# Performance work log

Measured on AMD Instinct MI355X. Metric: run time of the kernel, lower is better.

## Reference

```python
import jax, jax.numpy as jnp
import numpy as np

B = 8
C = 128          # channels
H = 1024         # sparse (hidden) channels in bottleneck
START = 128      # start_frames
SPARSE = 8192    # sparse_frames
K = 512          # k_sparse
N_UP = 6         # log2(SPARSE/START) upsample blocks
EPS = 1e-5


def conv1d(x, w, b, stride=1, pad=0):
    # x: (B, Cin, L), w: (Cout, Cin, K)
    y = jax.lax.conv_general_dilated(
        x, w, window_strides=(stride,), padding=[(pad, pad)],
        dimension_numbers=('NCW', 'OIW', 'NCW'))
    return y + b[None, :, None]


def batch_norm(x, g, beta):
    # training-mode BatchNorm1d: stats over (batch, length) per channel
    m = x.mean(axis=(0, 2), keepdims=True)
    v = x.var(axis=(0, 2), keepdims=True)
    return (x - m) * jax.lax.rsqrt(v + EPS) * g[None, :, None] + beta[None, :, None]


def lrelu(x):
    return jnp.where(x >= 0, x, 0.2 * x)


def setup_inputs() -> dict:
    key = jax.random.key(0)
    ks = jax.random.split(key, 16)
    s = 0.05
    return {
        'x': jax.random.normal(ks[0], (B, C, START), dtype=jnp.float32),
        'up_w': jax.random.normal(ks[1], (N_UP, C, C, 3), dtype=jnp.float32) * s,
        'up_b': jnp.zeros((N_UP, C), dtype=jnp.float32),
        'up_g': jnp.ones((N_UP, C), dtype=jnp.float32),
        'up_beta': jnp.zeros((N_UP, C), dtype=jnp.float32),
        'up_out_w': jax.random.normal(ks[2], (C, C, 3), dtype=jnp.float32) * s,
        'up_out_b': jnp.zeros((C,), dtype=jnp.float32),
        # SparseBottleneck 1x1 convs (stored as (out,in) matrices)
        'sb_up_w': jax.random.normal(ks[3], (H, C), dtype=jnp.float32) * s,
        'sb_up_b': jnp.zeros((H,), dtype=jnp.float32),
        'sal_w': jax.random.normal(ks[4], (H, C), dtype=jnp.float32) * s,
        'sal_b': jnp.zeros((H,), dtype=jnp.float32),
        'sb_down_w': jax.random.normal(ks[5], (C, H), dtype=jnp.float32) * s,
        'sb_down_b': jnp.zeros((C,), dtype=jnp.float32),
        'dn_w': jax.random.normal(ks[6], (3, C, C, 7), dtype=jnp.float32) * s,
        'dn_b': jnp.zeros((3, C), dtype=jnp.float32),
        'dn_g': jnp.ones((3, C), dtype=jnp.float32),
        'dn_beta': jnp.zeros((3, C), dtype=jnp.float32),
    }


def reference(x, up_w, up_b, up_g, up_beta, up_out_w, up_out_b,
              sb_up_w, sb_up_b, sal_w, sal_b, sb_down_w, sb_down_b,
              dn_w, dn_b, dn_g, dn_beta):
    # ---- ConvUpsample: 128 -> 8192 frames ----
    for i in range(N_UP):
        x = jnp.repeat(x, 2, axis=-1)
        x = conv1d(x, up_w[i], up_b[i], stride=1, pad=1)
        x = lrelu(batch_norm(x, up_g[i], up_beta[i]))
    x = conv1d(x, up_out_w, up_out_b, stride=1, pad=1)  # (B, C, 8192)

    # ---- SparseBottleneck ----
    sig = jnp.einsum('bcl,hc->bhl', x, sb_up_w) + sb_up_b[None, :, None]   # (B,H,L)
    sal = jnp.einsum('bcl,hc->bhl', x, sal_w) + sal_b[None, :, None]       # (B,H,L)
    flat = jax.nn.softmax(sal.reshape(B, -1), axis=-1)   # softmax over H*L
    vals, idx = jax.lax.top_k(flat, K)                   # (B, K)
    sparse = jnp.zeros_like(flat).at[jnp.arange(B)[:, None], idx].set(vals)
    sal = sparse.reshape(sal.shape)
    x = sig * sal                                         # gated, (B,H,L)
    x = jnp.einsum('bhl,ch->bcl', x, sb_down_w) + sb_down_b[None, :, None]

    # ---- down stack: 8192 -> 128 frames ----
    for i in range(3):
        x = conv1d(x, dn_w[i], dn_b[i], stride=4, pad=3)
        x = lrelu(x)
        x = batch_norm(x, dn_g[i], dn_beta[i])
    return x  # (B, C, 128)
```

## Files before the change

### kernel.cpp

```cpp
#include <hip/hip_runtime.h>
#include <hip/hip_bf16.h>


#define DEV_INLINE __device__ __forceinline__

constexpr int NB   = 8;
constexpr int NC   = 128;
constexpr int NH   = 1024;
constexpr int LFULL= 8192;
constexpr int KSEL = 512;
constexpr int CAP  = 32768;

typedef __attribute__((ext_vector_type(4))) float f32x4;
typedef __attribute__((ext_vector_type(8))) short bf16x8;

DEV_INLINE unsigned monoKey(float f) {
    unsigned u = __float_as_uint(f);
    return (u & 0x80000000u) ? ~u : (u | 0x80000000u);
}
DEV_INLINE float keyToF(unsigned k) {
    unsigned u = (k & 0x80000000u) ? (k ^ 0x80000000u) : ~k;
    return __uint_as_float(u);
}
DEV_INLINE unsigned monoKey16(unsigned u) {
    return (u & 0x8000u) ? ((~u) & 0xFFFFu) : (u | 0x8000u);
}
DEV_INLINE unsigned bf16r(float f) {
    unsigned u = __float_as_uint(f);
    return (u + 0x7FFFu + ((u >> 16) & 1u)) >> 16;
}
DEV_INLINE float lrelu(float v) { return v >= 0.f ? v : 0.2f * v; }
DEV_INLINE float f4c(const float4& v, int k) {
    return k == 0 ? v.x : k == 1 ? v.y : k == 2 ? v.z : v.w;
}
DEV_INLINE int swz4(int p) { return p ^ ((p >> 3) & 7); }

DEV_INLINE void loadg4(const float* __restrict__ rowp, int g0, int L, float* e) {
    if (g0 >= 0 && g0 + 4 <= L) {
        float4 v = *(const float4*)(rowp + g0);
        e[0] = v.x; e[1] = v.y; e[2] = v.z; e[3] = v.w;
    } else {
#pragma unroll
        for (int t = 0; t < 4; t++) {
            int g = g0 + t;
            e[t] = (g >= 0 && g < L) ? rowp[g] : 0.f;
        }
    }
}

__global__ __launch_bounds__(256) void prep_k(
    const float* __restrict__ up_w, const float* __restrict__ up_out_w,
    const float* __restrict__ dn_w, float* __restrict__ wprep)
{
    int idx = blockIdx.x * 256 + threadIdx.x;
    if (idx < 393216) {
        int layer = idx >> 16;
        int r0 = idx & 65535;
        int c = r0 >> 9, r = (r0 >> 7) & 3, o = r0 & 127;
        const float* wsrc = up_w + ((size_t)layer * 128 + o) * 384 + c * 3;
        float w0 = wsrc[0], w1 = wsrc[1], w2 = wsrc[2];
        wprep[idx] = (r == 0) ? w0 : (r == 1) ? (w1 + w2) : (r == 2) ? (w0 + w1) : w2;
    } else if (idx < 442368) {
        int r0 = idx - 393216;
        int c = r0 / 384, k = (r0 / 128) % 3, o = r0 & 127;
        wprep[idx] = up_out_w[((size_t)o * 128 + c) * 3 + k];
    } else {
        int r0 = idx - 442368;
        int layer = r0 / 114688;
        int r1 = r0 - layer * 114688;
        int c = r1 / 896, k = (r1 / 128) % 7, o = r1 & 127;
        wprep[idx] = dn_w[((size_t)layer * 128 + o) * 896 + c * 7 + k];
    }
}

__global__ __launch_bounds__(256) void prepA_k(
    const float* __restrict__ up_w, const float* __restrict__ up_out_w,
    unsigned short* __restrict__ afrag)
{
    int idx = blockIdx.x * 256 + threadIdx.x;
    if (idx >= 221184) return;
    int rid = idx >> 6, lane = idx & 63;
    const int r15 = lane & 15, g = lane >> 4;
    unsigned short vals[8];
    if (rid < 3072) {
        int L  = rid >> 9;
        int r0 = rid & 511;
        int f = r0 & 3, ks = (r0 >> 2) & 1, cc = (r0 >> 3) & 1;
        int wo = (r0 >> 4) & 1, half = (r0 >> 5) & 1, ptap = (r0 >> 6) & 3;
        int o = wo * 64 + f * 16 + r15;
        int cb = cc * 64 + ks * 32 + g * 8;
#pragma unroll
        for (int e = 0; e < 8; e++) {
            const float* ws = up_w + (((size_t)L * 128 + o) * 128 + (cb + e)) * 3;
            float w0 = ws[0], w1 = ws[1], w2 = ws[2];
            float v = (ptap == 0) ? w0 : (ptap == 1) ? (w1 + w2)
                    : (ptap == 2) ? (w0 + w1) : w2;
            unsigned hi = bf16r(v);
            if (half == 0) vals[e] = (unsigned short)hi;
            else vals[e] = (unsigned short)bf16r(v - __uint_as_float(hi << 16));
        }
    } else {
        int r2 = rid - 3072;
        int f = r2 & 3, ks = (r2 >> 2) & 1, cc = (r2 >> 3) & 1;
        int wo = (r2 >> 4) & 1, half = (r2 >> 5) & 1, tap = r2 >> 6;
        int o = wo * 64 + f * 16 + r15;
        int cb = cc * 64 + ks * 32 + g * 8;
#pragma unroll
        for (int e = 0; e < 8; e++) {
            float v = up_out_w[((size_t)o * 128 + (cb + e)) * 3 + tap];
            unsigned hi = bf16r(v);
            if (half == 0) vals[e] = (unsigned short)hi;
            else vals[e] = (unsigned short)bf16r(v - __uint_as_float(hi << 16));
        }
    }
    unsigned pk[4];
#pragma unroll
    for (int q = 0; q < 4; q++)
        pk[q] = (unsigned)vals[2*q] | ((unsigned)vals[2*q+1] << 16);
    *(uint4*)(afrag + (size_t)rid * 512 + lane * 8) = make_uint4(pk[0], pk[1], pk[2], pk[3]);
}

__global__ __launch_bounds__(256) void redstats_k(
    const float* __restrict__ partial, int nb, float* __restrict__ stats)
{
    const int c = threadIdx.x;
    float s0 = 0.f, s1 = 0.f, s2 = 0.f, s3 = 0.f;
    for (int i = blockIdx.x * 4; i < nb; i += gridDim.x * 4) {
        s0 += partial[(size_t)(i + 0) * 256 + c];
        s1 += partial[(size_t)(i + 1) * 256 + c];
        s2 += partial[(size_t)(i + 2) * 256 + c];
        s3 += partial[(size_t)(i + 3) * 256 + c];
    }
    float s = (s0 + s1) + (s2 + s3);
    if (s != 0.f || blockIdx.x == 0) atomicAdd(&stats[c], s);
}

template<int INMODE>
__global__ __launch_bounds__(512) void mconvU_k(
    const float* __restrict__ in, float* __restrict__ out,
    const unsigned short* __restrict__ afrag, const float* __restrict__ bias,
    const float* __restrict__ stp, const float* __restrict__ gp,
    const float* __restrict__ btp, float inv_n,
    float* __restrict__ partial, int L_in)
{
    __shared__ unsigned short Xh[66 * 64], Xl[66 * 64];
    __shared__ float scs[NC], shs[NC];
    __shared__ float sstat[256];

    const int b = blockIdx.y, tile0 = blockIdx.x * 64, tid = threadIdx.x;
    const int lane = tid & 63, wid = tid >> 6;
    const int wo = wid >> 2, par = (wid >> 1) & 1, jh = wid & 1;
    const int r15 = lane & 15, g = lane >> 4;
    const int bid = b * gridDim.x + blockIdx.x;

    if (tid < 256) sstat[tid] = 0.f;
    if (INMODE > 0) {
        for (int c = tid; c < NC; c += 512) {
            float m  = stp[c] * inv_n;
            float va = stp[NC + c] * inv_n - m * m;
            float sc = gp[c] * rsqrtf(va + 1e-5f);
            scs[c] = sc;
            shs[c] = btp[c] - m * sc;
        }
    }

    f32x4 acc[4][2];
#pragma unroll
    for (int i = 0; i < 4; i++)
#pragma unroll
        for (int j = 0; j < 2; j++) acc[i][j] = (f32x4)(0.f);

    for (int cc = 0; cc < 2; cc++) {
        __syncthreads();
        {
            int r = tid & 63;
            int l = tile0 - 1 + r;
            for (int c0 = (tid >> 6); c0 < 64; c0 += 8) {
                int c = cc * 64 + c0;
                float v = 0.f;
                if (l >= 0 && l < L_in) {
                    v = in[((size_t)b * NC + c) * L_in + l];
                    if (INMODE > 0) v = lrelu(v * scs[c] + shs[c]);
                }
                unsigned hi = bf16r(v);
                unsigned lo = bf16r(v - __uint_as_float(hi << 16));
                unsigned bo = ((unsigned)(r * 128 + c0 * 2)) ^ (((unsigned)(r & 7)) << 4);
                *(unsigned short*)((char*)Xh + bo) = (unsigned short)hi;
                *(unsigned short*)((char*)Xl + bo) = (unsigned short)lo;
            }
            if (tid < 128) {
                int r2 = 64 + (tid >> 6);
                int l2 = tile0 - 1 + r2;
                int c0 = tid & 63;
                int c = cc * 64 + c0;
                float v = 0.f;
                if (l2 >= 0 && l2 < L_in) {
                    v = in[((size_t)b * NC + c) * L_in + l2];
                    if (INMODE > 0) v = lrelu(v * scs[c] + shs[c]);
                }
                unsigned hi = bf16r(v);
                unsigned lo = bf16r(v - __uint_as_float(hi << 16));
                unsigned bo = ((unsigned)(r2 * 128 + c0 * 2)) ^ (((unsigned)(r2 & 7)) << 4);
                *(unsigned short*)((char*)Xh + bo) = (unsigned short)hi;
                *(unsigned short*)((char*)Xl + bo) = (unsigned short)lo;
            }
        }
        __syncthreads();
#pragma unroll
        for (int pt = 0; pt < 2; pt++) {
            const int ptap = par * 2 + pt;
            const int roff = (ptap == 0) ? 0 : (ptap == 3) ? 2 : 1;
#pragma unroll
            for (int combo = 0; combo < 3; combo++) {
                const int ah = (combo == 2) ? 1 : 0;
                const unsigned short* Xs = (combo == 1) ? Xl : Xh;
                bf16x8 af[8];
#pragma unroll
                for (int ks = 0; ks < 2; ks++)
#pragma unroll
                    for (int f = 0; f < 4; f++) {
                        int rec = ((((ptap * 2 + ah) * 2 + wo) * 2 + cc) * 2 + ks) * 4 + f;
                        af[ks * 4 + f] = *(const bf16x8*)(afrag + (size_t)rec * 512 + lane * 8);
                    }
#pragma unroll
                for (int ks = 0; ks < 2; ks++) {
                    bf16x8 bf_[2];
#pragma unroll
                    for (int j = 0; j < 2; j++) {
                        int row = (jh * 2 + j) * 16 + r15 + roff;
                        unsigned bo = ((unsigned)(row * 128 + ks * 64 + g * 16))
                                    ^ (((unsigned)(row & 7)) << 4);
                        bf_[j] = *(const bf16x8*)((const char*)Xs + bo);
                    }
#pragma unroll
                    for (int i = 0; i < 4; i++)
#pragma unroll
                        for (int j = 0; j < 2; j++)
                            acc[i][j] = __builtin_amdgcn_mfma_f32_16x16x32_bf16(
                                af[ks * 4 + i], bf_[j], acc[i][j], 0, 0, 0);
                }
            }
        }
    }

    const int L_out = 2 * L_in;
#pragma unroll
    for (int i = 0; i < 4; i++) {
#pragma unroll
        for (int r = 0; r < 4; r++) {
            const int o = wo * 64 + i * 16 + g * 4 + r;
            const float bv = bias[o];
            float s1 = 0.f, s2 = 0.f;
#pragma unroll
            for (int j = 0; j < 2; j++) {
                float v = acc[i][j][r] + bv;
                int lout = 2 * (tile0 + (jh * 2 + j) * 16 + r15) + par;
                out[((size_t)b * NC + o) * L_out + lout] = v;
                s1 += v; s2 += v * v;
            }
#pragma unroll
            for (int m = 1; m < 16; m <<= 1) {
                s1 += __shfl_xor(s1, m);
                s2 += __shfl_xor(s2, m);
            }
            if (r15 == 0) {
                atomicAdd(&sstat[o], s1);
                atomicAdd(&sstat[NC + o], s2);
            }
        }
    }
    __syncthreads();
    if (tid < 256) partial[(size_t)bid * 256 + tid] = sstat[tid];
}

__global__ __launch_bounds__(512) void mconvF_k(
    const float* __restrict__ in, float* __restrict__ out,
    const unsigned short* __restrict__ afrag, const float* __restrict__ bias,
    const float* __restrict__ stp, const float* __restrict__ gp,
    const float* __restrict__ btp, float inv_n,
    unsigned short* __restrict__ xtout)
{
    __shared__ unsigned short Xh[130 * 64], Xl[130 * 64];
    __shared__ float scs[NC], shs[NC];

    const int b = blockIdx.y, l0 = blockIdx.x * 128, tid = threadIdx.x;
    const int lane = tid & 63, wid = tid >> 6;
    const int wo = wid >> 2, wl = (wid & 3) * 32;
    const int r15 = lane & 15, g = lane >> 4;

    for (int c = tid; c < NC; c += 512) {
        float m  = stp[c] * inv_n;
        float va = stp[NC + c] * inv_n - m * m;
        float sc = gp[c] * rsqrtf(va + 1e-5f);
        scs[c] = sc;
        shs[c] = btp[c] - m * sc;
    }

    f32x4 acc[4][2];
#pragma unroll
    for (int i = 0; i < 4; i++)
#pragma unroll
        for (int j = 0; j < 2; j++) acc[i][j] = (f32x4)(0.f);

    for (int cc = 0; cc < 2; cc++) {
        __syncthreads();
        {
            int r = tid & 127;
            int l = l0 - 1 + r;
            for (int c0 = (tid >> 7); c0 < 64; c0 += 4) {
                int c = cc * 64 + c0;
                float v = 0.f;
                if (l >= 0 && l < LFULL) {
                    v = in[((size_t)b * NC + c) * LFULL + l];
                    v = lrelu(v * scs[c] + shs[c]);
                }
                unsigned hi = bf16r(v);
                unsigned lo = bf16r(v - __uint_as_float(hi << 16));
                unsigned bo = ((unsigned)(r * 128 + c0 * 2)) ^ (((unsigned)(r & 7)) << 4);
                *(unsigned short*)((char*)Xh + bo) = (unsigned short)hi;
                *(unsigned short*)((char*)Xl + bo) = (unsigned short)lo;
            }
            if (tid < 128) {
                int r2 = 128 + (tid >> 6);
                int l2 = l0 - 1 + r2;
                int c0 = tid & 63;
                int c = cc * 64 + c0;
                float v = 0.f;
                if (l2 >= 0 && l2 < LFULL) {
                    v = in[((size_t)b * NC + c) * LFULL + l2];
                    v = lrelu(v * scs[c] + shs[c]);
                }
                unsigned hi = bf16r(v);
                unsigned lo = bf16r(v - __uint_as_float(hi << 16));
                unsigned bo = ((unsigned)(r2 * 128 + c0 * 2)) ^ (((unsigned)(r2 & 7)) << 4);
                *(unsigned short*)((char*)Xh + bo) = (unsigned short)hi;
                *(unsigned short*)((char*)Xl + bo) = (unsigned short)lo;
            }
        }
        __syncthreads();
#pragma unroll
        for (int tap = 0; tap < 3; tap++) {
#pragma unroll
            for (int combo = 0; combo < 3; combo++) {
                const int ah = (combo == 2) ? 1 : 0;
                const unsigned short* Xs = (combo == 1) ? Xl : Xh;
                bf16x8 af[8];
#pragma unroll
                for (int ks = 0; ks < 2; ks++)
#pragma unroll
                    for (int f = 0; f < 4; f++) {
                        int rec = 3072 + ((((tap * 2 + ah) * 2 + wo) * 2 + cc) * 2 + ks) * 4 + f;
                        af[ks * 4 + f] = *(const bf16x8*)(afrag + (size_t)rec * 512 + lane * 8);
                    }
#pragma unroll
                for (int ks = 0; ks < 2; ks++) {
                    bf16x8 bf_[2];
#pragma unroll
                    for (int j = 0; j < 2; j++) {
                        int row = wl + j * 16 + r15 + tap;
                        unsigned bo = ((unsigned)(row * 128 + ks * 64 + g * 16))
                                    ^ (((unsigned)(row & 7)) << 4);
                        bf_[j] = *(const bf16x8*)((const char*)Xs + bo);
                    }
#pragma unroll
                    for (int i = 0; i < 4; i++)
#pragma unroll
                        for (int j = 0; j < 2; j++)
                            acc[i][j] = __builtin_amdgcn_mfma_f32_16x16x32_bf16(
                                af[ks * 4 + i], bf_[j], acc[i][j], 0, 0, 0);
                }
            }
        }
    }

#pragma unroll
    for (int i = 0; i < 4; i++) {
#pragma unroll
        for (int r = 0; r < 4; r++) {
            const int o = wo * 64 + i * 16 + g * 4 + r;
            const float bv = bias[o];
#pragma unroll
            for (int j = 0; j < 2; j++) {
                float v = acc[i][j][r] + bv;
                int l = l0 + wl + j * 16 + r15;
                out[((size_t)b * NC + o) * LFULL + l] = v;
                xtout[((size_t)b * LFULL + l) * NC + o] = (unsigned short)bf16r(v);
            }
        }
    }
}

template<int KW, int STRIDE, int PAD, bool UPS, int INMODE, bool OUTACT, bool STATS, int TT, bool XPOSE, int OCW>
__global__ __launch_bounds__(256) void conv7_k(
    const float* __restrict__ in, float* __restrict__ out,
    const float* __restrict__ wp, const float* __restrict__ bias,
    const float* __restrict__ stp, const float* __restrict__ gp,
    const float* __restrict__ btp, float inv_n,
    float* __restrict__ stats, unsigned short* __restrict__ xtout,
    int L_in, int L_out)
{
    constexpr int CC    = (KW == 7) ? 8 : 16;
    constexpr int PT    = 64 * TT;
    constexpr int TTO   = UPS ? 2 * TT : TT;
    constexpr int NWR   = UPS ? 4 : KW;
    constexpr int OCB   = 4 * OCW;
    constexpr int SPAN  = UPS ? (PT + 2) : ((PT - 1) * STRIDE + KW);
    constexpr int NCH   = (SPAN + 3) / 4;
    constexpr int NCH8  = (NCH + 7) & ~7;
    constexpr int XROW  = 4 * NCH8 + 4;
    constexpr int NLD   = (CC * NCH + 255) / 256;
    constexpr int XSPAN = UPS ? (TT + 2) : ((TT - 1) * STRIDE + KW);
    constexpr int STEP  = UPS ? TT : TT * STRIDE;
    constexpr int NWQ   = CC * NWR * (OCB / 4);
    static_assert((STEP & 3) == 0, "conv7 swizzle path requires STEP%4==0");
    static_assert(OCW == 4 || OCW == 8, "OCW must be 4 or 8");

    __shared__ float xs[CC][XROW];
    __shared__ float wls[CC * NWR * OCB];
    __shared__ float scs[NC], shs[NC];

    const int b = blockIdx.z, ocb = blockIdx.y, tid = threadIdx.x;
    const int t0 = blockIdx.x * PT, lane = tid & 63;
    const int wid = tid >> 6;
    const int oc0 = ocb * OCB + wid * OCW;
    const int gb = UPS ? (t0 - 1) : (t0 * STRIDE - PAD);

    if (INMODE > 0) {
        for (int c = tid; c < NC; c += 256) {
            float m  = stp[c] * inv_n;
            float va = stp[NC + c] * inv_n - m * m;
            float sc = gp[c] * rsqrtf(va + 1e-5f);
            scs[c] = sc;
            shs[c] = btp[c] - m * sc;
        }
        __syncthreads();
    }

    float acc[OCW][TTO];
#pragma unroll
    for (int i = 0; i < OCW; i++)
#pragma unroll
        for (int j = 0; j < TTO; j++) acc[i][j] = 0.f;

    float pre[NLD][4];

#define C7_STAGEW(CCBASE) do {                                              \
    for (int _u = tid; _u < NWQ; _u += 256) {                               \
        int _row = _u / (OCB / 4), _g8 = _u % (OCB / 4);                    \
        int _cl = _row / NWR, _t = _row % NWR;                              \
        ((float4*)wls)[_u] = *(const float4*)(wp +                          \
            ((size_t)((CCBASE) + _cl) * NWR + _t) * 128 + ocb * OCB + _g8 * 4); \
    }                                                                       \
} while (0)

#define C7_COMPCI(CI) do {                                                  \
    float _q[XSPAN];                                                        \
    const int _qb4 = lane * (STEP / 4);                                     \
    _Pragma("unroll")                                                       \
    for (int _u = 0; _u < XSPAN / 4; _u++) {                                \
        float4 _v = *(const float4*)&xs[CI][4 * swz4(_qb4 + _u)];           \
        _q[4*_u] = _v.x; _q[4*_u+1] = _v.y;                                 \
        _q[4*_u+2] = _v.z; _q[4*_u+3] = _v.w;                               \
    }                                                                       \
    if constexpr ((XSPAN & 3) != 0) {                                       \
        const int _pt = swz4(_qb4 + XSPAN / 4);                             \
        if constexpr ((XSPAN & 3) >= 2) {                                   \
            float2 _v = *(const float2*)&xs[CI][4 * _pt];                   \
            _q[(XSPAN & ~3)] = _v.x; _q[(XSPAN & ~3) + 1] = _v.y;           \
        }                                                                   \
        if constexpr ((XSPAN & 3) == 1)                                     \
            _q[XSPAN - 1] = xs[CI][4 * _pt];                                \
        else if constexpr ((XSPAN & 3) == 3)                                \
            _q[XSPAN - 1] = xs[CI][4 * _pt + 2];                            \
    }                                                                       \
    {                                                                       \
        _Pragma("unroll")                                                   \
        for (int _k = 0; _k < KW; _k++) {                                   \
            if constexpr (OCW == 8) {                                       \
                const float4 _w0 = *(const float4*)&wls[((CI) * NWR + _k) * OCB + wid * 8];     \
                const float4 _w1 = *(const float4*)&wls[((CI) * NWR + _k) * OCB + wid * 8 + 4]; \
                _Pragma("unroll")                                           \
                for (int _i = 0; _i < 8; _i++) {                            \
                    float _wv = f4c(_i < 4 ? _w0 : _w1, _i & 3);            \
                    _Pragma("unroll")                                       \
                    for (int _j = 0; _j < TT; _j++)                         \
                        acc[_i][_j] = fmaf(_wv, _q[_j * STRIDE + _k], acc[_i][_j]); \
                }                                                           \
            } else {                                                        \
                const float4 _w0 = *(const float4*)&wls[((CI) * NWR + _k) * OCB + wid * 4];     \
                _Pragma("unroll")                                           \
                for (int _i = 0; _i < 4; _i++) {                            \
                    float _wv = f4c(_w0, _i);                               \
                    _Pragma("unroll")                                       \
                    for (int _j = 0; _j < TT; _j++)                         \
                        acc[_i][_j] = fmaf(_wv, _q[_j * STRIDE + _k], acc[_i][_j]); \
                }                                                           \
            }                                                               \
        }                                                                   \
    }                                                                       \
} while (0)

#pragma unroll
    for (int u = 0; u < NLD; u++) {
        int idx = tid + u * 256;
        if (idx < CC * NCH) {
            int cl = idx / NCH, q = idx - cl * NCH;
            loadg4(in + ((size_t)b * NC + cl) * L_in, gb + 4 * q, L_in, pre[u]);
        }
    }
#pragma unroll
    for (int u = 0; u < NLD; u++) {
        int idx = tid + u * 256;
        if (idx < CC * NCH) {
            int cl = idx / NCH, q = idx - cl * NCH;
            int g0 = gb + 4 * q;
            float e[4];
#pragma unroll
            for (int t = 0; t < 4; t++) {
                float v = pre[u][t];
                if (INMODE > 0) {
                    int gg = g0 + t;
                    if (gg >= 0 && gg < L_in) {
                        float s = v * scs[cl] + shs[cl];
                        v = (INMODE == 2) ? lrelu(s) : s;
                    }
                }
                e[t] = v;
            }
            *(float4*)&xs[cl][4 * swz4(q)] = make_float4(e[0], e[1], e[2], e[3]);
        }
    }
    C7_STAGEW(0);
    __syncthreads();

    for (int cc = 0; cc < NC; cc += CC) {
        if (cc + CC < NC) {
#pragma unroll
            for (int u = 0; u < NLD; u++) {
                int idx = tid + u * 256;
                if (idx < CC * NCH) {
                    int cl = idx / NCH, q = idx - cl * NCH;
                    loadg4(in + ((size_t)b * NC + cc + CC + cl) * L_in,
                           gb + 4 * q, L_in, pre[u]);
                }
            }
        }
#pragma unroll
        for (int ci = 0; ci < CC; ci++) {
            C7_COMPCI(ci);
        }
        __syncthreads();
        if (cc + CC < NC) {
#pragma unroll
            for (int u = 0; u < NLD; u++) {
                int idx = tid + u * 256;
                if (idx < CC * NCH) {
                    int cl = idx / NCH, q = idx - cl * NCH;
                    int g0 = gb + 4 * q;
                    int c = cc + CC + cl;
                    float e[4];
#pragma unroll
                    for (int t = 0; t < 4; t++) {
                        float v = pre[u][t];
                        if (INMODE > 0) {
                            int gg = g0 + t;
                            if (gg >= 0 && gg < L_in) {
                                float s = v * scs[c] + shs[c];
                                v = (INMODE == 2) ? lrelu(s) : s;
                            }
                        }
                        e[t] = v;
                    }
                    *(float4*)&xs[cl][4 * swz4(q)] = make_float4(e[0], e[1], e[2], e[3]);
                }
            }
            C7_STAGEW(cc + CC);
            __syncthreads();
        }
    }
#undef C7_STAGEW
#undef C7_COMPCI

    const int po = t0 + lane * TTO;
#pragma unroll
    for (int i = 0; i < OCW; i++) {
        const int o = oc0 + i;
        const float bv = bias[o];
        float s1 = 0.f, s2 = 0.f;
        float tmpm[TTO];
#pragma unroll
        for (int j = 0; j < TTO; j++) {
            float v = acc[i][j] + bv;
            if (OUTACT) v = lrelu(v);
            tmpm[j] = v;
            if (STATS) { s1 += v; s2 += v * v; }
        }
        float* orow = out + ((size_t)b * NC + o) * L_out + po;
        if constexpr (TTO == 4)
            *(float4*)orow = make_float4(tmpm[0], tmpm[1], tmpm[2], tmpm[3]);
        else if constexpr (TTO == 2)
            *(float2*)orow = make_float2(tmpm[0], tmpm[1]);
        else
            orow[0] = tmpm[0];
        if (STATS) {
#pragma unroll
            for (int m = 1; m < 64; m <<= 1) {
                s1 += __shfl_xor(s1, m);
                s2 += __shfl_xor(s2, m);
            }
            if (lane == 0) {
                atomicAdd(&stats[o], s1);
                atomicAdd(&stats[NC + o], s2);
            }
        }
    }
}

__global__ __launch_bounds__(256) void cvtW_k(const float* __restrict__ W,
                                              unsigned short* __restrict__ Wbf)
{
    int i = blockIdx.x * 256 + threadIdx.x;
    const float4 a = *(const float4*)&W[i * 8];
    const float4 b = *(const float4*)&W[i * 8 + 4];
    unsigned pk[4];
    pk[0] = bf16r(a.x) | (bf16r(a.y) << 16);
    pk[1] = bf16r(a.z) | (bf16r(a.w) << 16);
    pk[2] = bf16r(b.x) | (bf16r(b.y) << 16);
    pk[3] = bf16r(b.z) | (bf16r(b.w) << 16);
    *(uint4*)&Wbf[i * 8] = make_uint4(pk[0], pk[1], pk[2], pk[3]);
}

template<int PHASE>
__global__ __launch_bounds__(256) void salM2_k(
    const unsigned short* __restrict__ xT, const unsigned short* __restrict__ Wbf,
    const float* __restrict__ bias, float* __restrict__ gsum,
    unsigned* __restrict__ ghist, const unsigned* __restrict__ thrv,
    unsigned* __restrict__ candcnt, unsigned* __restrict__ candI)
{
    __shared__ unsigned short Bls[128 * 128];
    __shared__ float redsm[4];

    const int b  = blockIdx.z;
    const int h0 = blockIdx.y * 128;
    const int l0 = blockIdx.x * 128;
    const int tid = threadIdx.x;
    const int lane = tid & 63;
    const int wid = tid >> 6;
    const int wh = (wid >> 1) * 64;
    const int wl = (wid & 1) * 64;
    const int r15 = lane & 15, g = lane >> 4;

    unsigned thr = 0;
    if (PHASE == 1) thr = thrv[b * 2];

    bf16x8 af[4][4];
#pragma unroll
    for (int ks = 0; ks < 4; ks++)
#pragma unroll
        for (int f = 0; f < 4; f++) {
            int row = h0 + wh + f * 16 + r15;
            af[ks][f] = *(const bf16x8*)(Wbf + (size_t)row * NC + ks * 32 + g * 8);
        }

    {
        const uint4* gB = (const uint4*)(xT + ((size_t)b * LFULL + l0) * NC);
        char* cB = (char*)Bls;
        for (int i = tid; i < 2048; i += 256) {
            int row = i >> 4, q = i & 15;
            unsigned sw = (unsigned)(row * 256 + q * 16) ^ (((unsigned)(row & 7)) << 4);
            *(uint4*)(cB + sw) = gB[i];
        }
    }
    __syncthreads();

    f32x4 acc[4][4];
#pragma unroll
    for (int i = 0; i < 4; i++)
#pragma unroll
        for (int j = 0; j < 4; j++) acc[i][j] = (f32x4)(0.f);

#pragma unroll
    for (int ks = 0; ks < 4; ks++) {
        bf16x8 bfv[4];
#pragma unroll
        for (int f = 0; f < 4; f++) {
            int rowB = wl + f * 16 + r15;
            unsigned offB = (unsigned)(rowB * 256 + ks * 64 + g * 16)
                          ^ (((unsigned)(rowB & 7)) << 4);
            bfv[f] = *(const bf16x8*)((const char*)Bls + offB);
        }
#pragma unroll
        for (int i = 0; i < 4; i++)
#pragma unroll
            for (int j = 0; j < 4; j++)
                acc[i][j] = __builtin_amdgcn_mfma_f32_16x16x32_bf16(
                    af[ks][i], bfv[j], acc[i][j], 0, 0, 0);
    }

    if constexpr (PHASE == 0) {
        __syncthreads();
        unsigned* lhist = (unsigned*)Bls;
        for (int i = tid; i < 8192; i += 256) lhist[i] = 0;
        __syncthreads();
        unsigned* myh = lhist + (tid & 1) * 4096;
        float expsum = 0.f;
#pragma unroll
        for (int i = 0; i < 4; i++) {
#pragma unroll
            for (int r = 0; r < 4; r++) {
                const int h = h0 + wh + i * 16 + g * 4 + r;
                const float bv = bias[h];
#pragma unroll
                for (int j = 0; j < 4; j++) {
                    float v = acc[i][j][r] + bv;
                    expsum += __expf(v);
                    atomicAdd(&myh[monoKey16(bf16r(v)) >> 4], 1u);
                }
            }
        }
#pragma unroll
        for (int m = 1; m < 64; m <<= 1) expsum += __shfl_xor(expsum, m);
        if (lane == 0) redsm[wid] = expsum;
        __syncthreads();
        for (int i = tid; i < 4096; i += 256) {
            unsigned s = lhist[i] + lhist[4096 + i];
            if (s) atomicAdd(&ghist[b * 4096 + i], s);
        }
        if (tid == 0)
            atomicAdd(&gsum[b], redsm[0] + redsm[1] + redsm[2] + redsm[3]);
    } else {
#pragma unroll
        for (int i = 0; i < 4; i++) {
#pragma unroll
            for (int r = 0; r < 4; r++) {
                const int h = h0 + wh + i * 16 + g * 4 + r;
                const float bv = bias[h];
#pragma unroll
                for (int j = 0; j < 4; j++) {
                    float v = acc[i][j][r] + bv;
                    bool pr = monoKey16(bf16r(v)) >= thr;
                    unsigned long long m = __ballot(pr);
                    if (m) {
                        int leader = __ffsll((unsigned long long)m) - 1;
                        int cnt = __popcll(m);
                        unsigned basepos = 0;
                        if (lane == leader)
                            basepos = atomicAdd(&candcnt[b], (unsigned)cnt);
                        basepos = __shfl(basepos, leader);
                        if (pr) {
                            int rr = __popcll(m & ((1ull << lane) - 1ull));
                            unsigned pos = basepos + (unsigned)rr;
                            if (pos < CAP) {
                                int l = l0 + wl + j * 16 + r15;
                                candI[b * CAP + pos] = (unsigned)((h << 13) | l);
                            }
                        }
                    }
                }
            }
        }
    }
}

__global__ __launch_bounds__(256) void scan2_k(
    const unsigned* __restrict__ ghist, unsigned* __restrict__ thrv)
{
    const int b = blockIdx.x, tid = threadIdx.x;
    __shared__ unsigned part[256];
    unsigned s = 0;
#pragma unroll
    for (int i = 0; i < 16; i++) s += ghist[b * 4096 + tid * 16 + i];
    part[tid] = s;
    __syncthreads();
    if (tid == 0) {
        unsigned cum = 0; int ch;
        for (ch = 255; ch >= 0; ch--) {
            if (cum + part[ch] >= KSEL) break;
            cum += part[ch];
        }
        int bin = 0;
        if (ch >= 0) {
            for (bin = ch * 16 + 15; bin > ch * 16; bin--) {
                unsigned c = ghist[b * 4096 + bin];
                if (cum + c >= KSEL) break;
                cum += c;
            }
        }
        int bcol = bin > 0 ? bin - 1 : 0;
        thrv[b * 2] = (unsigned)bcol << 4;
    }
}

__global__ __launch_bounds__(128) void recompute_k(
    const unsigned* __restrict__ candcnt, const unsigned* __restrict__ candI,
    const float* __restrict__ xu, const float* __restrict__ W,
    const float* __restrict__ bias, unsigned* __restrict__ candK)
{
    const int b = blockIdx.y;
    const unsigned cnt = min(candcnt[b], (unsigned)CAP);
    const int t = threadIdx.x;
    __shared__ float wsum[2];
    for (unsigned k = blockIdx.x; k < cnt; k += 1024) {
        unsigned e = candI[b * CAP + k];
        int h = e >> 13, l = e & 8191;
        float prod = W[h * NC + t] * xu[(b * NC + t) * LFULL + l];
#pragma unroll
        for (int m = 1; m < 64; m <<= 1) prod += __shfl_xor(prod, m);
        if ((t & 63) == 0) wsum[t >> 6] = prod;
        __syncthreads();
        if (t == 0) candK[b * CAP + k] = monoKey(wsum[0] + wsum[1] + bias[h]);
        __syncthreads();
    }
}

__global__ __launch_bounds__(256) void select2_k(
    const unsigned* __restrict__ candcnt, const unsigned* __restrict__ candK,
    const unsigned* __restrict__ candI,
    uint2* __restrict__ selected, unsigned* __restrict__ selcnt)
{
    const int b = blockIdx.x, tid = threadIdx.x;
    __shared__ unsigned h1[4096];
    __shared__ unsigned l2k[2048], l2i[2048];
    __shared__ unsigned part[256];
    __shared__ unsigned sh[8];

    const unsigned Nc = min(candcnt[b], (unsigned)CAP);
    const unsigned* kk = candK + b * CAP;
    const unsigned* ii = candI + b * CAP;
    uint2* sel = selected + b * KSEL;

    for (int i = tid; i < 4096; i += 256) h1[i] = 0;
    if (tid < 8) sh[tid] = 0;
    __syncthreads();
    for (unsigned i = tid; i < Nc; i += 256) atomicAdd(&h1[kk[i] >> 20], 1u);
    __syncthreads();
    {
        unsigned s = 0;
#pragma unroll
        for (int i = 0; i < 16; i++) s += h1[tid * 16 + i];
        part[tid] = s;
        __syncthreads();
        if (tid == 0) {
            unsigned cum = 0; int ch;
            for (ch = 255; ch >= 0; ch--) { if (cum + part[ch] >= KSEL) break; cum += part[ch]; }
            int bin = 0;
            if (ch >= 0)
                for (bin = ch * 16 + 15; bin > ch * 16; bin--) {
                    unsigned c = h1[bin];
                    if (cum + c >= KSEL) break;
                    cum += c;
                }
            sh[2] = (unsigned)bin; sh[3] = KSEL - cum;
        }
    }
    __syncthreads();
    const unsigned b1 = sh[2], need1 = sh[3];
    for (int i = tid; i < 1024; i += 256) h1[i] = 0;
    __syncthreads();
    for (unsigned i = tid; i < Nc; i += 256) {
        unsigned k = kk[i], bin = k >> 20;
        if (bin > b1) {
            unsigned p = atomicAdd(&sh[0], 1u);
            if (p < KSEL) sel[p] = make_uint2(k, ii[i]);
        } else if (bin == b1) {
            atomicAdd(&h1[(k >> 10) & 1023], 1u);
        }
    }
    __syncthreads();
    {
        unsigned s = 0;
#pragma unroll
        for (int i = 0; i < 4; i++) s += h1[tid * 4 + i];
        part[tid] = s;
        __syncthreads();
        if (tid == 0) {
            unsigned cum = 0; int ch;
            for (ch = 255; ch >= 0; ch--) { if (cum + part[ch] >= need1) break; cum += part[ch]; }
            int bin = 0;
            if (ch >= 0)
                for (bin = ch * 4 + 3; bin > ch * 4; bin--) {
                    unsigned c = h1[bin];
                    if (cum + c >= need1) break;
                    cum += c;
                }
            sh[4] = (unsigned)bin; sh[5] = need1 - cum;
        }
    }
    __syncthreads();
    const unsigned b2 = sh[4], need2 = sh[5];
    for (int i = tid; i < 1024; i += 256) h1[i] = 0;
    __syncthreads();
    for (unsigned i = tid; i < Nc; i += 256) {
        unsigned k = kk[i];
        if ((k >> 20) != b1) continue;
        unsigned mb = (k >> 10) & 1023;
        if (mb > b2) {
            unsigned p = atomicAdd(&sh[0], 1u);
            if (p < KSEL) sel[p] = make_uint2(k, ii[i]);
        } else if (mb == b2) {
            unsigned j = atomicAdd(&sh[1], 1u);
            if (j < 2048) { l2k[j] = k; l2i[j] = ii[i]; atomicAdd(&h1[k & 1023], 1u); }
        }
    }
    __syncthreads();
    const unsigned m2 = min(sh[1], 2048u);
    {
        unsigned s = 0;
#pragma unroll
        for (int i = 0; i < 4; i++) s += h1[tid * 4 + i];
        part[tid] = s;
        __syncthreads();
        if (tid == 0) {
            unsigned cum = 0; int ch;
            for (ch = 255; ch >= 0; ch--) { if (cum + part[ch] >= need2) break; cum += part[ch]; }
            int bin = 0;
            if (ch >= 0)
                for (bin = ch * 4 + 3; bin > ch * 4; bin--) {
                    unsigned c = h1[bin];
                    if (cum + c >= need2) break;
                    cum += c;
                }
            sh[6] = (unsigned)bin; sh[7] = need2 - cum;
        }
    }
    __syncthreads();
    const unsigned b3 = sh[6], need3 = sh[7];
    if (tid == 0) sh[1] = 0;
    __syncthreads();
    for (unsigned i = tid; i < m2; i += 256) {
        unsigned k = l2k[i], lb = k & 1023;
        if (lb > b3) {
            unsigned p = atomicAdd(&sh[0], 1u);
            if (p < KSEL) sel[p] = make_uint2(k, l2i[i]);
        } else if (lb == b3) {
            unsigned t = atomicAdd(&sh[1], 1u);
            if (t < need3) {
                unsigned p = atomicAdd(&sh[0], 1u);
                if (p < KSEL) sel[p] = make_uint2(k, l2i[i]);
            }
        }
    }
    __syncthreads();
    if (tid == 0) selcnt[b] = min(sh[0], (unsigned)KSEL);
}

__global__ __launch_bounds__(128) void scatter2_k(
    const uint2* __restrict__ selected, const unsigned* __restrict__ selcnt,
    const float* __restrict__ gsum, const float* __restrict__ xu,
    const float* __restrict__ upw, const float* __restrict__ upb,
    float* __restrict__ gval)
{
    const int b = blockIdx.y, kidx = blockIdx.x;
    if (kidx >= (int)selcnt[b]) return;
    const uint2 s = selected[b * KSEL + kidx];
    const float salv = keyToF(s.x);
    const unsigned idx = s.y;
    const int h = idx >> 13, l = idx & 8191;
    const int t = threadIdx.x;

    float prod = upw[h * NC + t] * xu[(b * NC + t) * LFULL + l];
#pragma unroll
    for (int m = 1; m < 64; m <<= 1) prod += __shfl_xor(prod, m);
    __shared__ float wsum[2];
    if ((t & 63) == 0) wsum[t >> 6] = prod;
    __syncthreads();
    if (t == 0) {
        const float sig = wsum[0] + wsum[1] + upb[h];
        gval[b * KSEL + kidx] = sig * (__expf(salv) / gsum[b]);
    }
}

__global__ __launch_bounds__(128) void dnconst_k(
    const float* __restrict__ dn_w, const float* __restrict__ dnb,
    const float* __restrict__ dn_b0, float* __restrict__ cst)
{
    const int o = threadIdx.x;
    float accA = 0.f, accE = 0.f;
    for (int c = 0; c < NC; c++) {
        const float bv = dnb[c];
        const float* wp = dn_w + ((size_t)o * NC + c) * 7;
#pragma unroll
        for (int k = 0; k < 7; k++) {
            float w = wp[k];
            accA += w * bv;
            if (k >= 3) accE += w * bv;
        }
    }
    cst[o]       = accA + dn_b0[o];
    cst[NC + o]  = accE + dn_b0[o];
}

__global__ __launch_bounds__(256) void fillpre_k(
    const float* __restrict__ cst, float* __restrict__ pre)
{
    const int row = blockIdx.x;
    const int o = row & 127;
    const float vI = cst[o], v0 = cst[NC + o];
    float4* p = (float4*)(pre + (size_t)row * 2048);
#pragma unroll
    for (int u = 0; u < 2; u++) {
        int q = threadIdx.x + u * 256;
        float4 v = make_float4(vI, vI, vI, vI);
        if (q == 0) v.x = v0;
        p[q] = v;
    }
}

__global__ __launch_bounds__(128) void corrdn_k(
    const uint2* __restrict__ selected, const unsigned* __restrict__ selcnt,
    const float* __restrict__ gval, const float* __restrict__ dww,
    const float* __restrict__ w0p, float* __restrict__ pre)
{
    const int b = blockIdx.y, kidx = blockIdx.x;
    if (kidx >= (int)selcnt[b]) return;
    const unsigned idx = selected[b * KSEL + kidx].y;
    const int h = idx >> 13, l = idx & 8191;
    const float g = gval[b * KSEL + kidx];
    const int o = threadIdx.x;

    __shared__ float dlt[NC];
    dlt[o] = dww[o * NH + h] * g;
    __syncthreads();

    const int tlo = (l <= 3) ? 0 : ((l - 3 + 3) >> 2);
    const int thi = min(2047, (l + 3) >> 2);
    for (int t = tlo; t <= thi; t++) {
        const int k = l - 4 * t + 3;
        float corr = 0.f;
#pragma unroll 4
        for (int c = 0; c < NC; c++)
            corr += w0p[(size_t)c * 896 + k * 128 + o] * dlt[c];
        atomicAdd(&pre[((size_t)b * NC + o) * 2048 + t], corr);
    }
}

__global__ __launch_bounds__(256) void actstats_k(
    float* __restrict__ pre, float* __restrict__ stats)
{
    const int row = blockIdx.x;
    const int o = row & 127;
    float4* p = (float4*)(pre + (size_t)row * 2048);
    float s1 = 0.f, s2 = 0.f;
#pragma unroll
    for (int u = 0; u < 2; u++) {
        int q = threadIdx.x + u * 256;
        float4 v = p[q];
        float e[4] = {v.x, v.y, v.z, v.w};
#pragma unroll
        for (int t = 0; t < 4; t++) {
            float a = lrelu(e[t]);
            e[t] = a;
            s1 += a; s2 += a * a;
        }
        p[q] = make_float4(e[0], e[1], e[2], e[3]);
    }
#pragma unroll
    for (int m = 1; m < 64; m <<= 1) {
        s1 += __shfl_xor(s1, m);
        s2 += __shfl_xor(s2, m);
    }
    __shared__ float red[8];
    const int lane = threadIdx.x & 63, wid = threadIdx.x >> 6;
    if (lane == 0) { red[wid] = s1; red[4 + wid] = s2; }
    __syncthreads();
    if (threadIdx.x == 0) {
        atomicAdd(&stats[o],      red[0] + red[1] + red[2] + red[3]);
        atomicAdd(&stats[NC + o], red[4] + red[5] + red[6] + red[7]);
    }
}

__global__ void apply_k(const float* __restrict__ in, const float* __restrict__ stats,
                        const float* __restrict__ g, const float* __restrict__ bt,
                        float* __restrict__ out, float inv_n)
{
    int i = blockIdx.x * 256 + threadIdx.x;
    int c = (i >> 7) & 127;
    float m  = stats[c] * inv_n;
    float va = stats[NC + c] * inv_n - m * m;
    float sc = g[c] * rsqrtf(va + 1e-5f);
    out[i] = in[i] * sc + (bt[c] - m * sc);
}

extern "C" void kernel_launch(void* const* d_in, const int* in_sizes, int n_in,
                              void* d_out, int out_size, void* d_ws, size_t ws_size,
                              hipStream_t stream)
{
    const float* x        = (const float*)d_in[0];
    const float* up_w     = (const float*)d_in[1];
    const float* up_b     = (const float*)d_in[2];
    const float* up_g     = (const float*)d_in[3];
    const float* up_beta  = (const float*)d_in[4];
    const float* up_out_w = (const float*)d_in[5];
    const float* up_out_b = (const float*)d_in[6];
    const float* sb_up_w  = (const float*)d_in[7];
    const float* sb_up_b  = (const float*)d_in[8];
    const float* sal_w    = (const float*)d_in[9];
    const float* sal_b    = (const float*)d_in[10];
    const float* sb_dn_w  = (const float*)d_in[11];
    const float* sb_dn_b  = (const float*)d_in[12];
    const float* dn_w     = (const float*)d_in[13];
    const float* dn_b     = (const float*)d_in[14];
    const float* dn_g     = (const float*)d_in[15];
    const float* dn_beta  = (const float*)d_in[16];

    char* ws = (char*)d_ws;
    float*          stats    = (float*)(ws + 0);
    float*          gsum     = (float*)(ws + 16384);
    unsigned*       thrv     = (unsigned*)(ws + 16416);
    unsigned*       candcnt  = (unsigned*)(ws + 16480);
    unsigned*       selcnt   = (unsigned*)(ws + 16512);
    uint2*          selected = (uint2*)(ws + 16640);
    unsigned*       ghist    = (unsigned*)(ws + 49408);
    unsigned*       candK    = (unsigned*)(ws + 180480);
    unsigned*       candI    = (unsigned*)(ws + 1229056);
    unsigned short* Wbf      = (unsigned short*)(ws + 2277632);
    float*          wprep    = (float*)(ws + 2539776);
    float*          B0       = (float*)(ws + 5685504);
    float*          B1       = (float*)(ws + 39239936);
    unsigned short* xT       = (unsigned short*)(ws + 72794368);
    unsigned short* Afrag    = (unsigned short*)(ws + 117440512);
    float*          partial  = (float*)(ws + 121634816);
    float*          gval     = (float*)(ws + 122159104);
    float*          cst      = (float*)(ws + 122175488);

    hipMemsetAsync(d_ws, 0, 16544, stream);
    hipMemsetAsync(ws + 49408, 0, 131072, stream);

    cvtW_k<<<64,256,0,stream>>>(sal_w, Wbf);
    prep_k<<<3072,256,0,stream>>>(up_w, up_out_w, dn_w, wprep);
    prepA_k<<<864,256,0,stream>>>(up_w, up_out_w, Afrag);

    mconvU_k<0><<<dim3(2,NB),512,0,stream>>>(
        x, B0, Afrag, up_b, nullptr, nullptr, nullptr, 0.f, partial, 128);
    redstats_k<<<16,256,0,stream>>>(partial, 2*NB, stats);
    mconvU_k<2><<<dim3(4,NB),512,0,stream>>>(
        B0, B1, Afrag + 1*262144, up_b + NC,
        stats, up_g, up_beta, 1.f/(float)(NB*256), partial, 256);
    redstats_k<<<16,256,0,stream>>>(partial, 4*NB, stats + 256);
    mconvU_k<2><<<dim3(8,NB),512,0,stream>>>(
        B1, B0, Afrag + 2*262144, up_b + 2*NC,
        stats + 256, up_g + NC, up_beta + NC, 1.f/(float)(NB*512), partial, 512);
    redstats_k<<<16,256,0,stream>>>(partial, 8*NB, stats + 2*256);
    mconvU_k<2><<<dim3(16,NB),512,0,stream>>>(
        B0, B1, Afrag + 3*262144, up_b + 3*NC,
        stats + 2*256, up_g + 2*NC, up_beta + 2*NC, 1.f/(float)(NB*1024), partial, 1024);
    redstats_k<<<16,256,0,stream>>>(partial, 16*NB, stats + 3*256);
    mconvU_k<2><<<dim3(32,NB),512,0,stream>>>(
        B1, B0, Afrag + 4*262144, up_b + 4*NC,
        stats + 3*256, up_g + 3*NC, up_beta + 3*NC, 1.f/(float)(NB*2048), partial, 2048);
    redstats_k<<<16,256,0,stream>>>(partial, 32*NB, stats + 4*256);
    mconvU_k<2><<<dim3(64,NB),512,0,stream>>>(
        B0, B1, Afrag + 5*262144, up_b + 5*NC,
        stats + 4*256, up_g + 4*NC, up_beta + 4*NC, 1.f/(float)(NB*4096), partial, 4096);
    redstats_k<<<16,256,0,stream>>>(partial, 64*NB, stats + 5*256);
    mconvF_k<<<dim3(64,NB),512,0,stream>>>(
        B1, B0, Afrag, up_out_b,
        stats + 5*256, up_g + 5*NC, up_beta + 5*NC, 1.f/(float)(NB*LFULL), xT);

    salM2_k<0><<<dim3(64,8,NB),256,0,stream>>>(xT, Wbf, sal_b, gsum, ghist,
                                               nullptr, nullptr, nullptr);
    scan2_k<<<NB,256,0,stream>>>(ghist, thrv);
    salM2_k<1><<<dim3(64,8,NB),256,0,stream>>>(xT, Wbf, sal_b, nullptr, nullptr,
                                               thrv, candcnt, candI);
    recompute_k<<<dim3(1024,NB),128,0,stream>>>(candcnt, candI, B0, sal_w, sal_b, candK);
    select2_k<<<NB,256,0,stream>>>(candcnt, candK, candI, selected, selcnt);
    scatter2_k<<<dim3(KSEL,NB),128,0,stream>>>(selected, selcnt, gsum, B0,
                                               sb_up_w, sb_up_b, gval);

    dnconst_k<<<1,128,0,stream>>>(dn_w, sb_dn_b, dn_b, cst);
    fillpre_k<<<NB*NC,256,0,stream>>>(cst, B1);
    corrdn_k<<<dim3(KSEL,NB),128,0,stream>>>(selected, selcnt, gval, sb_dn_w,
                                             wprep + 442368, B1);
    actstats_k<<<NB*NC,256,0,stream>>>(B1, stats + 6*256);

    conv7_k<7,4,3,false,1,true,true,1,false,4><<<dim3(8,8,NB),256,0,stream>>>(
        B1, B0, wprep + 442368 + 114688, dn_b + NC,
        stats + 6*256, dn_g, dn_beta, 1.f/(float)(NB*2048),
        stats + 7*256, nullptr, 2048, 512);
    conv7_k<7,4,3,false,1,true,true,1,false,4><<<dim3(2,8,NB),256,0,stream>>>(
        B0, B1, wprep + 442368 + 2*114688, dn_b + 2*NC,
        stats + 7*256, dn_g + NC, dn_beta + NC, 1.f/(float)(NB*512),
        stats + 8*256, nullptr, 512, 128);

    apply_k<<<(out_size + 255)/256,256,0,stream>>>(
        B1, stats + 8*256, dn_g + 2*NC, dn_beta + 2*NC, (float*)d_out,
        1.f/(float)(NB*128));
}
```

Baseline: 649.1 us.

## Replace second saliency GEMM pass with per-tile local top-K candidate buffering

The saliency GEMM used to run twice: once for the histogram and softmax sum, then again to collect candidates above the global threshold. Now each tile builds its own histogram, picks a tile-local threshold that keeps at least K entries, and stores those keyed candidates in a per-tile buffer. A light filter kernel then applies the global threshold to the buffered entries instead of recomputing the GEMM. This adds per-tile shared-memory scans and extra global writes, and a tile that overflows its TCAP buffer can silently drop candidates.

```diff
diff --git a/kernel.cpp b/kernel.cpp
--- a/kernel.cpp
+++ b/kernel.cpp
@@ -10,6 +10,7 @@
 constexpr int LFULL= 8192;
 constexpr int KSEL = 512;
 constexpr int CAP  = 32768;
+constexpr int TCAP = 2048;
 
 typedef __attribute__((ext_vector_type(4))) float f32x4;
 typedef __attribute__((ext_vector_type(8))) short bf16x8;
@@ -630,15 +631,16 @@
     *(uint4*)&Wbf[i * 8] = make_uint4(pk[0], pk[1], pk[2], pk[3]);
 }
 
-template<int PHASE>
-__global__ __launch_bounds__(256) void salM2_k(
+__global__ __launch_bounds__(256) void salM3_k(
     const unsigned short* __restrict__ xT, const unsigned short* __restrict__ Wbf,
     const float* __restrict__ bias, float* __restrict__ gsum,
-    unsigned* __restrict__ ghist, const unsigned* __restrict__ thrv,
-    unsigned* __restrict__ candcnt, unsigned* __restrict__ candI)
+    unsigned* __restrict__ ghist, unsigned* __restrict__ tcand,
+    unsigned* __restrict__ tcnt)
 {
     __shared__ unsigned short Bls[128 * 128];
     __shared__ float redsm[4];
+    __shared__ unsigned part[256];
+    __shared__ unsigned shv[2];
 
     const int b  = blockIdx.z;
     const int h0 = blockIdx.y * 128;
@@ -649,9 +651,7 @@
     const int wh = (wid >> 1) * 64;
     const int wl = (wid & 1) * 64;
     const int r15 = lane & 15, g = lane >> 4;
-
-    unsigned thr = 0;
-    if (PHASE == 1) thr = thrv[b * 2];
+    const int tileid = (b * 8 + blockIdx.y) * 64 + blockIdx.x;
 
     bf16x8 af[4][4];
 #pragma unroll
@@ -697,65 +697,130 @@
                     af[ks][i], bfv[j], acc[i][j], 0, 0, 0);
     }
 
-    if constexpr (PHASE == 0) {
-        __syncthreads();
-        unsigned* lhist = (unsigned*)Bls;
-        for (int i = tid; i < 8192; i += 256) lhist[i] = 0;
-        __syncthreads();
-        unsigned* myh = lhist + (tid & 1) * 4096;
-        float expsum = 0.f;
-#pragma unroll
-        for (int i = 0; i < 4; i++) {
-#pragma unroll
-            for (int r = 0; r < 4; r++) {
-                const int h = h0 + wh + i * 16 + g * 4 + r;
-                const float bv = bias[h];
-#pragma unroll
-                for (int j = 0; j < 4; j++) {
-                    float v = acc[i][j][r] + bv;
-                    expsum += __expf(v);
-                    atomicAdd(&myh[monoKey16(bf16r(v)) >> 4], 1u);
-                }
-            }
-        }
-#pragma unroll
-        for (int m = 1; m < 64; m <<= 1) expsum += __shfl_xor(expsum, m);
-        if (lane == 0) redsm[wid] = expsum;
-        __syncthreads();
-        for (int i = tid; i < 4096; i += 256) {
-            unsigned s = lhist[i] + lhist[4096 + i];
-            if (s) atomicAdd(&ghist[b * 4096 + i], s);
-        }
-        if (tid == 0)
-            atomicAdd(&gsum[b], redsm[0] + redsm[1] + redsm[2] + redsm[3]);
-    } else {
-#pragma unroll
-        for (int i = 0; i < 4; i++) {
-#pragma unroll
-            for (int r = 0; r < 4; r++) {
-                const int h = h0 + wh + i * 16 + g * 4 + r;
-                const float bv = bias[h];
-#pragma unroll
-                for (int j = 0; j < 4; j++) {
-                    float v = acc[i][j][r] + bv;
-                    bool pr = monoKey16(bf16r(v)) >= thr;
-                    unsigned long long m = __ballot(pr);
-                    if (m) {
-                        int leader = __ffsll((unsigned long long)m) - 1;
-                        int cnt = __popcll(m);
-                        unsigned basepos = 0;
-                        if (lane == leader)
-                            basepos = atomicAdd(&candcnt[b], (unsigned)cnt);
-                        basepos = __shfl(basepos, leader);
-                        if (pr) {
-                            int rr = __popcll(m & ((1ull << lane) - 1ull));
-                            unsigned pos = basepos + (unsigned)rr;
-                            if (pos < CAP) {
-                                int l = l0 + wl + j * 16 + r15;
-                                candI[b * CAP + pos] = (unsigned)((h << 13) | l);
-                            }
+    __syncthreads();
+    unsigned* hA = (unsigned*)Bls;
+    for (int i = tid; i < 8192; i += 256) hA[i] = 0;
+    if (tid < 2) shv[tid] = 0;
+    __syncthreads();
+    unsigned* myh = hA + (tid & 1) * 4096;
+    float expsum = 0.f;
+#pragma unroll
+    for (int i = 0; i < 4; i++) {
+#pragma unroll
+        for (int r = 0; r < 4; r++) {
+            const int h = h0 + wh + i * 16 + g * 4 + r;
+            const float bv = bias[h];
+#pragma unroll
+            for (int j = 0; j < 4; j++) {
+                float v = acc[i][j][r] + bv;
+                expsum += __expf(v);
+                atomicAdd(&myh[monoKey16(bf16r(v)) >> 4], 1u);
+            }
+        }
+    }
+#pragma unroll
+    for (int m = 1; m < 64; m <<= 1) expsum += __shfl_xor(expsum, m);
+    if (lane == 0) redsm[wid] = expsum;
+    __syncthreads();
+    for (int i = tid; i < 4096; i += 256) {
+        unsigned s = hA[i] + hA[4096 + i];
+        hA[i] = s;
+        if (s) atomicAdd(&ghist[b * 4096 + i], s);
+    }
+    __syncthreads();
+    {
+        unsigned s = 0;
+#pragma unroll
+        for (int i = 0; i < 16; i++) s += hA[tid * 16 + i];
+        part[tid] = s;
+    }
+    __syncthreads();
+    if (tid == 0) {
+        atomicAdd(&gsum[b], redsm[0] + redsm[1] + redsm[2] + redsm[3]);
+        unsigned cum = 0; int ch;
+        for (ch = 255; ch >= 0; ch--) {
+            if (cum + part[ch] >= KSEL) break;
+            cum += part[ch];
+        }
+        int bin = 0;
+        if (ch >= 0) {
+            for (bin = ch * 16 + 15; bin > ch * 16; bin--) {
+                unsigned c = hA[bin];
+                if (cum + c >= KSEL) break;
+                cum += c;
+            }
+        }
+        shv[0] = (unsigned)(bin > 0 ? bin - 1 : 0) << 4;
+    }
+    __syncthreads();
+    const unsigned lthr = shv[0];
+    unsigned* tc = tcand + (size_t)tileid * TCAP;
+#pragma unroll
+    for (int i = 0; i < 4; i++) {
+#pragma unroll
+        for (int r = 0; r < 4; r++) {
+            const int hl = wh + i * 16 + g * 4 + r;
+            const float bv = bias[h0 + hl];
+#pragma unroll
+            for (int j = 0; j < 4; j++) {
+                float v = acc[i][j][r] + bv;
+                unsigned k16 = monoKey16(bf16r(v));
+                bool pr = k16 >= lthr;
+                unsigned long long m = __ballot(pr);
+                if (m) {
+                    int leader = __ffsll((unsigned long long)m) - 1;
+                    int cnt = __popcll(m);
+                    unsigned base = 0;
+                    if (lane == leader) base = atomicAdd(&shv[1], (unsigned)cnt);
+                    base = __shfl(base, leader);
+                    if (pr) {
+                        int rr = __popcll(m & ((1ull << lane) - 1ull));
+                        unsigned p = base + (unsigned)rr;
+                        if (p < TCAP) {
+                            int ll = wl + j * 16 + r15;
+                            tc[p] = (k16 << 16) | ((unsigned)hl << 7) | (unsigned)ll;
                         }
                     }
+                }
+            }
+        }
+    }
+    __syncthreads();
+    if (tid == 0) tcnt[tileid] = min(shv[1], (unsigned)TCAP);
+}
+
+__global__ __launch_bounds__(256) void filter_k(
+    const unsigned* __restrict__ tcand, const unsigned* __restrict__ tcnt,
+    const unsigned* __restrict__ thrv,
+    unsigned* __restrict__ candcnt, unsigned* __restrict__ candI)
+{
+    const int b = blockIdx.y, t = blockIdx.x;
+    const int tileid = b * 512 + t;
+    const unsigned thr = thrv[b * 2];
+    const unsigned cnt = tcnt[tileid];
+    const int h0 = (t >> 6) * 128, l0 = (t & 63) * 128;
+    const unsigned* tc = tcand + (size_t)tileid * TCAP;
+    const int lane = threadIdx.x & 63;
+
+    const unsigned n = (cnt + 255u) & ~255u;
+    for (unsigned i = threadIdx.x; i < n; i += 256) {
+        bool act = i < cnt;
+        unsigned e = act ? tc[i] : 0u;
+        bool pr = act && ((e >> 16) >= thr);
+        unsigned long long m = __ballot(pr);
+        if (m) {
+            int leader = __ffsll((unsigned long long)m) - 1;
+            int c = __popcll(m);
+            unsigned base = 0;
+            if (lane == leader) base = atomicAdd(&candcnt[b], (unsigned)c);
+            base = __shfl(base, leader);
+            if (pr) {
+                int rr = __popcll(m & ((1ull << lane) - 1ull));
+                unsigned p = base + (unsigned)rr;
+                if (p < CAP) {
+                    int h = h0 + (int)((e >> 7) & 127u);
+                    int l = l0 + (int)(e & 127u);
+                    candI[b * CAP + p] = (unsigned)((h << 13) | l);
                 }
             }
         }
@@ -1122,6 +1187,8 @@
     float*          partial  = (float*)(ws + 121634816);
     float*          gval     = (float*)(ws + 122159104);
     float*          cst      = (float*)(ws + 122175488);
+    unsigned*       tcnt     = (unsigned*)(ws + 122176512);
+    unsigned*       tcand    = (unsigned*)(ws + 125829120);
 
     hipMemsetAsync(d_ws, 0, 16544, stream);
     hipMemsetAsync(ws + 49408, 0, 131072, stream);
@@ -1157,11 +1224,10 @@
         B1, B0, Afrag, up_out_b,
         stats + 5*256, up_g + 5*NC, up_beta + 5*NC, 1.f/(float)(NB*LFULL), xT);
 
-    salM2_k<0><<<dim3(64,8,NB),256,0,stream>>>(xT, Wbf, sal_b, gsum, ghist,
-                                               nullptr, nullptr, nullptr);
+    salM3_k<<<dim3(64,8,NB),256,0,stream>>>(xT, Wbf, sal_b, gsum, ghist,
+                                            tcand, tcnt);
     scan2_k<<<NB,256,0,stream>>>(ghist, thrv);
-    salM2_k<1><<<dim3(64,8,NB),256,0,stream>>>(xT, Wbf, sal_b, nullptr, nullptr,
-                                               thrv, candcnt, candI);
+    filter_k<<<dim3(512,NB),256,0,stream>>>(tcand, tcnt, thrv, candcnt, candI);
     recompute_k<<<dim3(1024,NB),128,0,stream>>>(candcnt, candI, B0, sal_w, sal_b, candK);
     select2_k<<<NB,256,0,stream>>>(candcnt, candK, candI, selected, selcnt);
     scatter2_k<<<dim3(KSEL,NB),128,0,stream>>>(selected, selcnt, gsum, B0,
```

Result: slower. 719.9 us (+10.9%).
